# Optimization experiments

Hardware: AMD Instinct MI355X
Metric: run time of the kernel (lower is better)

The kernel has to match this reference:

```python
import jax, jax.numpy as jnp
import numpy as np

B, D_IN, D_H, D_OUT, E = 8192, 512, 2048, 512, 8


def setup_inputs() -> dict:
    key = jax.random.key(0)
    k = jax.random.split(key, 6)
    return {
        "x": jax.random.normal(k[0], (B, D_IN), dtype=jnp.float32),
        "groups": jax.random.randint(k[1], (B, 1), 0, E, dtype=jnp.int64),
        "W1": jax.random.normal(k[2], (E, D_IN, D_H), dtype=jnp.float32) * (1.0 / np.sqrt(D_IN)),
        "b1": jnp.zeros((E, D_H), dtype=jnp.float32),
        "W2": jax.random.normal(k[3], (E, D_H, D_OUT), dtype=jnp.float32) * (1.0 / np.sqrt(D_H)),
        "b2": jnp.zeros((E, D_OUT), dtype=jnp.float32),
    }


def reference(x, groups, W1, b1, W2, b2):
    # SubnetGate: hard one-hot routing on group column 0, then weighted
    # combine (gate value is exactly 1.0 for the selected expert).
    n_expert = W1.shape[0]
    gate = jax.nn.one_hot(groups[:, 0], n_expert, dtype=x.dtype)  # [B, E]
    out = jnp.zeros((x.shape[0], W2.shape[-1]), dtype=x.dtype)
    # Loop over the small fixed expert set (structurally distinct subnets);
    # mask-combine reproduces dispatch -> subnet -> scatter/combine exactly.
    for e in range(n_expert):
        h = jax.nn.relu(x @ W1[e] + b1[e])        # [B, D_H]
        y = h @ W2[e] + b2[e]                      # [B, D_OUT]
        out = out + gate[:, e:e + 1] * y
    return out
```

## Files before the change

### kernel.cpp

```cpp
#include <hip/hip_runtime.h>
#include <hip/hip_bf16.h>

typedef unsigned short u16;
typedef __bf16 bf16x8 __attribute__((ext_vector_type(8)));
typedef float floatx4 __attribute__((ext_vector_type(4)));
typedef unsigned short ushort8 __attribute__((ext_vector_type(8)));

#define GLOBAL_AS(p) ((const __attribute__((address_space(1))) void*)(p))
#define LDS_AS(p) ((__attribute__((address_space(3))) void*)(p))

constexpr int NB = 8192;
constexpr int DIN = 512;
constexpr int DH = 2048;
constexpr int DOUT = 512;
constexpr int NEXP = 8;
constexpr int ROWCAP = NB + NEXP * 128;
constexpr int RCAPRD = NB + NEXP * 256;
constexpr int TILE = 8192;

__device__ __forceinline__ u16 f2bf(float f) {
    unsigned u = __builtin_bit_cast(unsigned, f);
    unsigned r = u + 0x7FFFu + ((u >> 16) & 1u);
    return (u16)(r >> 16);
}

__device__ __forceinline__ int slot_off(int row, int kl) {
    return row * 64 + ((((kl >> 3) ^ (row & 7)) << 3) | (kl & 7));
}

__global__ void route_kernel(const int* __restrict__ groups, int* __restrict__ cnt,
                             int* __restrict__ offs, int* __restrict__ perm,
                             int* __restrict__ rpos) {
    __shared__ int wc[NEXP * 4];
    __shared__ int lcur[NEXP * 4];
    int t = threadIdx.x;
    int w = t >> 6;
    if (t < NEXP * 4) wc[t] = 0;
    __syncthreads();
    for (int i = t; i < NB; i += 256) atomicAdd(&wc[groups[i] * 4 + w], 1);
    __syncthreads();
    if (t == 0) {
        int run = 0;
        for (int e = 0; e < NEXP; ++e) {
            offs[e] = run;
            int s = run;
            for (int j = 0; j < 4; ++j) { lcur[e * 4 + j] = s; s += wc[e * 4 + j]; }
            cnt[e] = s - run;
            run += (((s - run) + 127) >> 7) << 7;
        }
    }
    __syncthreads();
    for (int i = t; i < NB; i += 256) {
        int e = groups[i];
        int pos = atomicAdd(&lcur[e * 4 + w], 1);
        perm[pos] = i;
        rpos[i] = pos;
    }
}

__global__ __launch_bounds__(256) void prep_kernel(
        const float* __restrict__ x, const float* __restrict__ W1,
        const float* __restrict__ W2, const int* __restrict__ rpos,
        u16* __restrict__ xsT, u16* __restrict__ w1tT, u16* __restrict__ w2tT) {
    int bx = blockIdx.x;
    int t = threadIdx.x;
    if (bx < 4096) {
        __shared__ float tile[64][65];
        bool isW1 = bx < 2048;
        int b = isW1 ? bx : bx - 2048;
        int e = b >> 8;
        int q = b & 255;
        int C = isW1 ? DH : DOUT;
        int NTP = C >> 7;
        int KTP = isW1 ? (DIN >> 6) : (DH >> 6);
        int rt = isW1 ? (q >> 5) : (q >> 3);
        int ct = isW1 ? (q & 31) : (q & 7);
        const float* s = (isW1 ? W1 : W2) + (size_t)e * (isW1 ? DIN * DH : DH * DOUT);
        u16* d = isW1 ? w1tT : w2tT;
        int r0 = rt * 64, c0 = ct * 64;
        for (int i = 0; i < 4; ++i) {
            int r = (t >> 4) + i * 16;
            int c = (t & 15) * 4;
            const float4 v = *(const float4*)&s[(size_t)(r0 + r) * C + c0 + c];
            tile[r][c] = v.x; tile[r][c + 1] = v.y; tile[r][c + 2] = v.z; tile[r][c + 3] = v.w;
        }
        __syncthreads();
        for (int i = 0; i < 4; ++i) {
            int c = (t >> 4) + i * 16;
            int r = (t & 15) * 4;
            int n = c0 + c, k = r0 + r;
            ushort4 o;
            o.x = f2bf(tile[r][c]); o.y = f2bf(tile[r + 1][c]);
            o.z = f2bf(tile[r + 2][c]); o.w = f2bf(tile[r + 3][c]);
            size_t off = ((size_t)(e * NTP + (n >> 7)) * KTP + (k >> 6)) * TILE
                         + slot_off(n & 127, k & 63);
            *(ushort4*)&d[off] = o;
        }
    } else {
        int r = t >> 6, lane = t & 63;
        int i = (bx - 4096) * 4 + r;
        int pos = rpos[i];
        int k = lane * 8;
        const float4 a = *(const float4*)&x[(size_t)i * DIN + k];
        const float4 b = *(const float4*)&x[(size_t)i * DIN + k + 4];
        ushort8 o;
        o[0] = f2bf(a.x); o[1] = f2bf(a.y); o[2] = f2bf(a.z); o[3] = f2bf(a.w);
        o[4] = f2bf(b.x); o[5] = f2bf(b.y); o[6] = f2bf(b.z); o[7] = f2bf(b.w);
        int lp = pos & 127;
        size_t off = (size_t)(pos >> 7) * 8 * TILE + (size_t)(k >> 6) * TILE
                     + slot_off(lp, k & 63);
        *(ushort8*)&xsT[off] = o;
    }
}


#define LDF(base, row, c0) \
    (*(const bf16x8*)&(base)[(row) * 64 + ((((c0) ^ ((row) & 7))) << 3)])

__device__ __forceinline__ void stage3(const u16* a0, const u16* a1, const u16* b,
                                       u16* buf, int soff, int doff) {
    __builtin_amdgcn_global_load_lds(GLOBAL_AS(a0 + soff), LDS_AS(buf + doff), 16, 0, 0);
    __builtin_amdgcn_global_load_lds(GLOBAL_AS(a0 + 4096 + soff), LDS_AS(buf + 4096 + doff), 16, 0, 0);
    __builtin_amdgcn_global_load_lds(GLOBAL_AS(a1 + soff), LDS_AS(buf + TILE + doff), 16, 0, 0);
    __builtin_amdgcn_global_load_lds(GLOBAL_AS(a1 + 4096 + soff), LDS_AS(buf + TILE + 4096 + doff), 16, 0, 0);
    __builtin_amdgcn_global_load_lds(GLOBAL_AS(b + soff), LDS_AS(buf + 2 * TILE + doff), 16, 0, 0);
    __builtin_amdgcn_global_load_lds(GLOBAL_AS(b + 4096 + soff), LDS_AS(buf + 2 * TILE + 4096 + doff), 16, 0, 0);
}

__device__ __forceinline__ void compute_step(const u16* At, const u16* Bt,
                                             int arow, int brow,
                                             floatx4 (&acc)[4][4], int q, int li) {
#pragma unroll
    for (int s = 0; s < 2; ++s) {
        int c0 = s * 4 + q;
        bf16x8 bfr[4];
#pragma unroll
        for (int fn = 0; fn < 4; ++fn) bfr[fn] = LDF(Bt, brow + fn * 16 + li, c0);
#pragma unroll
        for (int fm = 0; fm < 4; ++fm) {
            bf16x8 af = LDF(At, arow + fm * 16 + li, c0);
#pragma unroll
            for (int fn = 0; fn < 4; ++fn)
                acc[fm][fn] = __builtin_amdgcn_mfma_f32_16x16x32_bf16(
                    af, bfr[fn], acc[fm][fn], 0, 0, 0);
        }
    }
}

__global__ __launch_bounds__(512) __attribute__((amdgpu_waves_per_eu(2)))
void gemm_a(const u16* __restrict__ At, const u16* __restrict__ Bt,
            const float* __restrict__ bias, u16* __restrict__ hsT,
            const int* __restrict__ cnt, const int* __restrict__ offs) {
    __shared__ u16 sm[2 * 3 * TILE];
    int bx = blockIdx.x;
    int e = bx & 7;
    int r = bx >> 3;
    int nt = r & 15;
    int mt0 = r >> 4;
    int count = cnt[e];
    int base128 = offs[e] >> 7;
    int tid = threadIdx.x;
    int w = tid >> 6, l = tid & 63, q = l >> 4, li = l & 15;
    int wm = w >> 1, wn = w & 1;
    int aslot = wm >> 1, arow = (wm & 1) * 64, brow = wn * 64;
    int soff = tid * 8, doff = w * 512;
#pragma unroll 1
    for (int mt = mt0; mt * 256 < count; mt += 5) {
        const u16* a0 = At + (size_t)((base128 + mt * 2 + 0) * 8) * TILE;
        const u16* a1 = At + (size_t)((base128 + mt * 2 + 1) * 8) * TILE;
        const u16* b0 = Bt + (size_t)((e * 16 + nt) * 8) * TILE;
        floatx4 acc[4][4];
#pragma unroll
        for (int a = 0; a < 4; ++a)
#pragma unroll
            for (int b = 0; b < 4; ++b) acc[a][b] = (floatx4)0.0f;

        stage3(a0, a1, b0, sm, soff, doff);
        __syncthreads();
        int cur = 0;
#pragma unroll 1
        for (int kt = 0; kt < 8; ++kt) {
            if (kt + 1 < 8)
                stage3(a0 + (kt + 1) * TILE, a1 + (kt + 1) * TILE, b0 + (kt + 1) * TILE,
                       sm + (cur ^ 1) * 3 * TILE, soff, doff);
            const u16* Atile = sm + (size_t)(cur * 3 + aslot) * TILE;
            const u16* Btile = sm + (size_t)(cur * 3 + 2) * TILE;
            compute_step(Atile, Btile, arow, brow, acc, q, li);
            __syncthreads();
            cur ^= 1;
        }

        float bv[4];
#pragma unroll
        for (int fn = 0; fn < 4; ++fn)
            bv[fn] = bias[(size_t)e * DH + nt * 128 + wn * 64 + fn * 16 + li];
        u16* img = sm + (size_t)w * 4096;
#pragma unroll
        for (int fm = 0; fm < 4; ++fm)
#pragma unroll
            for (int fn = 0; fn < 4; ++fn)
#pragma unroll
                for (int rr = 0; rr < 4; ++rr) {
                    float v = acc[fm][fn][rr] + bv[fn];
                    v = v > 0.0f ? v : 0.0f;
                    int row = fm * 16 + q * 4 + rr;
                    int col = fn * 16 + li;
                    img[row * 64 + ((((col >> 3) ^ (row & 7)) << 3) | (col & 7))] = f2bf(v);
                }
        if ((mt * 2 + aslot) * 128 < count) {
            u16* dst = hsT + ((size_t)(base128 + mt * 2 + aslot) * 32 + nt * 2 + wn) * TILE
                       + (wm & 1) * 4096;
#pragma unroll
            for (int j = 0; j < 8; ++j)
                *(ushort8*)&dst[j * 512 + l * 8] = *(const ushort8*)&img[j * 512 + l * 8];
        }
        __syncthreads();
    }
}

__global__ __launch_bounds__(512) __attribute__((amdgpu_waves_per_eu(2)))
void gemm_b(const u16* __restrict__ At, const u16* __restrict__ Bt,
            float* __restrict__ ps, const int* __restrict__ cnt,
            const int* __restrict__ offs) {
    __shared__ u16 sm[2 * 3 * TILE];
    int bx = blockIdx.x;
    int e = bx & 7;
    int r = bx >> 3;
    int nt = r & 3;
    int ks = (r >> 2) & 1;
    int mt0 = r >> 3;
    int count = cnt[e];
    int seg = offs[e];
    int base128 = seg >> 7;
    int tid = threadIdx.x;
    int w = tid >> 6, l = tid & 63, q = l >> 4, li = l & 15;
    int wm = w >> 1, wn = w & 1;
    int aslot = wm >> 1, arow = (wm & 1) * 64, brow = wn * 64;
    int soff = tid * 8, doff = w * 512;
#pragma unroll 1
    for (int mt = mt0; mt * 256 < count; mt += 5) {
        const u16* a0 = At + (size_t)((base128 + mt * 2 + 0) * 32 + ks * 16) * TILE;
        const u16* a1 = At + (size_t)((base128 + mt * 2 + 1) * 32 + ks * 16) * TILE;
        const u16* b0 = Bt + (size_t)((e * 4 + nt) * 32 + ks * 16) * TILE;
        floatx4 acc[4][4];
#pragma unroll
        for (int a = 0; a < 4; ++a)
#pragma unroll
            for (int b = 0; b < 4; ++b) acc[a][b] = (floatx4)0.0f;

        stage3(a0, a1, b0, sm, soff, doff);
        __syncthreads();
        int cur = 0;
#pragma unroll 1
        for (int kt = 0; kt < 16; ++kt) {
            if (kt + 1 < 16)
                stage3(a0 + (kt + 1) * TILE, a1 + (kt + 1) * TILE, b0 + (kt + 1) * TILE,
                       sm + (cur ^ 1) * 3 * TILE, soff, doff);
            const u16* Atile = sm + (size_t)(cur * 3 + aslot) * TILE;
            const u16* Btile = sm + (size_t)(cur * 3 + 2) * TILE;
            compute_step(Atile, Btile, arow, brow, acc, q, li);
            __syncthreads();
            cur ^= 1;
        }

        if ((mt * 2 + aslot) * 128 < count) {
            float* pbase = ps + ((size_t)ks * ROWCAP + seg + (size_t)mt * 256) * DOUT;
#pragma unroll
            for (int fn = 0; fn < 4; ++fn) {
                int col = nt * 128 + wn * 64 + fn * 16 + li;
#pragma unroll
                for (int fm = 0; fm < 4; ++fm) {
                    int row0 = wm * 64 + fm * 16 + q * 4;
#pragma unroll
                    for (int rr = 0; rr < 4; ++rr)
                        pbase[(size_t)(row0 + rr) * DOUT + col] = acc[fm][fn][rr];
                }
            }
        }
    }
}

__global__ __launch_bounds__(256) void reduce_b(
        const float* __restrict__ ps, const int* __restrict__ rpos,
        const int* __restrict__ groups, const float* __restrict__ b2,
        float* __restrict__ out) {
    int idx = blockIdx.x * 256 + threadIdx.x;
    int i = idx >> 7;
    int c = (idx & 127) * 4;
    int pos = rpos[i];
    int g = groups[i];
    const float4 v0 = *(const float4*)&ps[(size_t)pos * DOUT + c];
    const float4 v1 = *(const float4*)&ps[((size_t)ROWCAP + pos) * DOUT + c];
    const float4 bb = *(const float4*)&b2[(size_t)g * DOUT + c];
    float4 o;
    o.x = v0.x + v1.x + bb.x; o.y = v0.y + v1.y + bb.y;
    o.z = v0.z + v1.z + bb.z; o.w = v0.w + v1.w + bb.w;
    *(float4*)&out[(size_t)i * DOUT + c] = o;
}

extern "C" void kernel_launch(void* const* d_in, const int* in_sizes, int n_in,
                              void* d_out, int out_size, void* d_ws, size_t ws_size,
                              hipStream_t stream) {
    const float* x = (const float*)d_in[0];
    const int* groups = (const int*)d_in[1];
    const float* W1 = (const float*)d_in[2];
    const float* b1 = (const float*)d_in[3];
    const float* W2 = (const float*)d_in[4];
    const float* b2 = (const float*)d_in[5];
    float* out = (float*)d_out;

    char* ws = (char*)d_ws;
    size_t o = 0;
    auto alloc = [&](size_t bytes) {
        void* p = ws + o;
        o = (o + bytes + 255) & ~(size_t)255;
        return p;
    };
    int* cnt = (int*)alloc(NEXP * 4);
    int* offs = (int*)alloc(NEXP * 4);
    int* perm = (int*)alloc((size_t)ROWCAP * 4);
    int* rpos = (int*)alloc((size_t)NB * 4);
    u16* xsT = (u16*)alloc((size_t)(RCAPRD / 128) * 8 * TILE * 2);
    u16* w1tT = (u16*)alloc((size_t)NEXP * DIN * DH * 2);
    u16* w2tT = (u16*)alloc((size_t)NEXP * DH * DOUT * 2);
    u16* hsT = (u16*)alloc((size_t)(RCAPRD / 128) * 32 * TILE * 2);
    float* ps = (float*)alloc((size_t)2 * ROWCAP * DOUT * 4);

    route_kernel<<<1, 256, 0, stream>>>(groups, cnt, offs, perm, rpos);
    prep_kernel<<<6144, 256, 0, stream>>>(x, W1, W2, rpos, xsT, w1tT, w2tT);
    gemm_a<<<NEXP * 16 * 5, 512, 0, stream>>>(xsT, w1tT, b1, hsT, cnt, offs);
    gemm_b<<<NEXP * 4 * 2 * 5, 512, 0, stream>>>(hsT, w2tT, ps, cnt, offs);
    reduce_b<<<(NB * (DOUT / 4)) / 256, 256, 0, stream>>>(ps, rpos, groups, b2, out);
}
```

Baseline: 228.2 us.

## Triple-buffer LDS pipeline with explicit vmcnt waits and shrink grid to 4 m-strides

Replaces the double-buffered K loop in both grouped GEMMs with a three-stage LDS ring that prefetches two tiles ahead. Explicit s_waitcnt vmcnt counts and raw s_barrier calls take the place of __syncthreads. LDS grows to 9 tiles (144KB) per block, which may cap occupancy at one block per CU. The grid's m-tile stride changes from 5 to 4 so the block count matches, and gemm_b gains a trailing barrier before the next m-tile reuses LDS.

Result: no change. 229.7 us (+0.7%).

```diff
diff --git a/kernel.cpp b/kernel.cpp
--- a/kernel.cpp
+++ b/kernel.cpp
@@ -147,11 +147,41 @@
     }
 }
 
+template <int KT>
+__device__ __forceinline__ void gemm_core3(const u16* a0, const u16* a1, const u16* b0,
+                                           u16* sm, floatx4 (&acc)[4][4],
+                                           int aslot, int arow, int brow,
+                                           int q, int li, int soff, int doff) {
+    stage3(a0, a1, b0, sm, soff, doff);
+    stage3(a0 + TILE, a1 + TILE, b0 + TILE, sm + 3 * TILE, soff, doff);
+    int cur = 0;
+#pragma unroll 1
+    for (int kt = 0; kt < KT; ++kt) {
+        if (kt + 2 < KT) {
+            int nb = cur + 2; if (nb >= 3) nb -= 3;
+            stage3(a0 + (size_t)(kt + 2) * TILE, a1 + (size_t)(kt + 2) * TILE,
+                   b0 + (size_t)(kt + 2) * TILE, sm + (size_t)nb * 3 * TILE, soff, doff);
+            asm volatile("s_waitcnt vmcnt(12)" ::: "memory");
+        } else if (kt + 1 < KT) {
+            asm volatile("s_waitcnt vmcnt(6)" ::: "memory");
+        } else {
+            asm volatile("s_waitcnt vmcnt(0)" ::: "memory");
+        }
+        __builtin_amdgcn_s_barrier();
+        __builtin_amdgcn_sched_barrier(0);
+        const u16* At = sm + (size_t)(cur * 3 + aslot) * TILE;
+        const u16* Bt = sm + (size_t)(cur * 3 + 2) * TILE;
+        compute_step(At, Bt, arow, brow, acc, q, li);
+        __builtin_amdgcn_s_barrier();
+        cur = (cur == 2) ? 0 : cur + 1;
+    }
+}
+
 __global__ __launch_bounds__(512) __attribute__((amdgpu_waves_per_eu(2)))
 void gemm_a(const u16* __restrict__ At, const u16* __restrict__ Bt,
             const float* __restrict__ bias, u16* __restrict__ hsT,
             const int* __restrict__ cnt, const int* __restrict__ offs) {
-    __shared__ u16 sm[2 * 3 * TILE];
+    __shared__ u16 sm[3 * 3 * TILE];
     int bx = blockIdx.x;
     int e = bx & 7;
     int r = bx >> 3;
@@ -165,7 +195,7 @@
     int aslot = wm >> 1, arow = (wm & 1) * 64, brow = wn * 64;
     int soff = tid * 8, doff = w * 512;
 #pragma unroll 1
-    for (int mt = mt0; mt * 256 < count; mt += 5) {
+    for (int mt = mt0; mt * 256 < count; mt += 4) {
         const u16* a0 = At + (size_t)((base128 + mt * 2 + 0) * 8) * TILE;
         const u16* a1 = At + (size_t)((base128 + mt * 2 + 1) * 8) * TILE;
         const u16* b0 = Bt + (size_t)((e * 16 + nt) * 8) * TILE;
@@ -175,20 +205,7 @@
 #pragma unroll
             for (int b = 0; b < 4; ++b) acc[a][b] = (floatx4)0.0f;
 
-        stage3(a0, a1, b0, sm, soff, doff);
-        __syncthreads();
-        int cur = 0;
-#pragma unroll 1
-        for (int kt = 0; kt < 8; ++kt) {
-            if (kt + 1 < 8)
-                stage3(a0 + (kt + 1) * TILE, a1 + (kt + 1) * TILE, b0 + (kt + 1) * TILE,
-                       sm + (cur ^ 1) * 3 * TILE, soff, doff);
-            const u16* Atile = sm + (size_t)(cur * 3 + aslot) * TILE;
-            const u16* Btile = sm + (size_t)(cur * 3 + 2) * TILE;
-            compute_step(Atile, Btile, arow, brow, acc, q, li);
-            __syncthreads();
-            cur ^= 1;
-        }
+        gemm_core3<8>(a0, a1, b0, sm, acc, aslot, arow, brow, q, li, soff, doff);
 
         float bv[4];
 #pragma unroll
@@ -222,7 +239,7 @@
 void gemm_b(const u16* __restrict__ At, const u16* __restrict__ Bt,
             float* __restrict__ ps, const int* __restrict__ cnt,
             const int* __restrict__ offs) {
-    __shared__ u16 sm[2 * 3 * TILE];
+    __shared__ u16 sm[3 * 3 * TILE];
     int bx = blockIdx.x;
     int e = bx & 7;
     int r = bx >> 3;
@@ -238,7 +255,7 @@
     int aslot = wm >> 1, arow = (wm & 1) * 64, brow = wn * 64;
     int soff = tid * 8, doff = w * 512;
 #pragma unroll 1
-    for (int mt = mt0; mt * 256 < count; mt += 5) {
+    for (int mt = mt0; mt * 256 < count; mt += 4) {
         const u16* a0 = At + (size_t)((base128 + mt * 2 + 0) * 32 + ks * 16) * TILE;
         const u16* a1 = At + (size_t)((base128 + mt * 2 + 1) * 32 + ks * 16) * TILE;
         const u16* b0 = Bt + (size_t)((e * 4 + nt) * 32 + ks * 16) * TILE;
@@ -248,20 +265,7 @@
 #pragma unroll
             for (int b = 0; b < 4; ++b) acc[a][b] = (floatx4)0.0f;
 
-        stage3(a0, a1, b0, sm, soff, doff);
-        __syncthreads();
-        int cur = 0;
-#pragma unroll 1
-        for (int kt = 0; kt < 16; ++kt) {
-            if (kt + 1 < 16)
-                stage3(a0 + (kt + 1) * TILE, a1 + (kt + 1) * TILE, b0 + (kt + 1) * TILE,
-                       sm + (cur ^ 1) * 3 * TILE, soff, doff);
-            const u16* Atile = sm + (size_t)(cur * 3 + aslot) * TILE;
-            const u16* Btile = sm + (size_t)(cur * 3 + 2) * TILE;
-            compute_step(Atile, Btile, arow, brow, acc, q, li);
-            __syncthreads();
-            cur ^= 1;
-        }
+        gemm_core3<16>(a0, a1, b0, sm, acc, aslot, arow, brow, q, li, soff, doff);
 
         if ((mt * 2 + aslot) * 128 < count) {
             float* pbase = ps + ((size_t)ks * ROWCAP + seg + (size_t)mt * 256) * DOUT;
@@ -277,6 +281,7 @@
                 }
             }
         }
+        __syncthreads();
     }
 }
 
@@ -328,7 +333,7 @@
 
     route_kernel<<<1, 256, 0, stream>>>(groups, cnt, offs, perm, rpos);
     prep_kernel<<<6144, 256, 0, stream>>>(x, W1, W2, rpos, xsT, w1tT, w2tT);
-    gemm_a<<<NEXP * 16 * 5, 512, 0, stream>>>(xsT, w1tT, b1, hsT, cnt, offs);
-    gemm_b<<<NEXP * 4 * 2 * 5, 512, 0, stream>>>(hsT, w2tT, ps, cnt, offs);
+    gemm_a<<<NEXP * 16 * 4, 512, 0, stream>>>(xsT, w1tT, b1, hsT, cnt, offs);
+    gemm_b<<<NEXP * 4 * 2 * 4, 512, 0, stream>>>(hsT, w2tT, ps, cnt, offs);
     reduce_b<<<(NB * (DOUT / 4)) / 256, 256, 0, stream>>>(ps, rpos, groups, b2, out);
 }
```
